# Kernel optimization log

Measured on AMD Instinct MI355X. Metric: run time of the kernel, lower is better.

The kernel has to match this reference:

```python
import jax, jax.numpy as jnp
import numpy as np

N_NODES = 50000
N_EDGES = 800000
EDGE_DIM = 64
HID = 64


def setup_inputs() -> dict:
    key = jax.random.key(0)
    ks = jax.random.split(key, 8)
    hidden_atom_emb = jax.random.normal(ks[0], (N_NODES, HID), dtype=jnp.float32)
    edge_emb = jax.random.normal(ks[1], (N_EDGES, EDGE_DIM), dtype=jnp.float32)
    edge_list = jax.random.randint(ks[2], (N_EDGES, 2), 0, N_NODES, dtype=jnp.int64)
    # filter MLP params (xavier-uniform-like scaling)
    lim1 = float(np.sqrt(6.0 / (EDGE_DIM + HID)))
    W1 = jax.random.uniform(ks[3], (EDGE_DIM, HID), minval=-lim1, maxval=lim1, dtype=jnp.float32)
    b1 = jnp.zeros((HID,), dtype=jnp.float32)
    lim2 = float(np.sqrt(6.0 / (HID + HID)))
    W2 = jax.random.uniform(ks[4], (HID, HID), minval=-lim2, maxval=lim2, dtype=jnp.float32)
    b2 = jnp.zeros((HID,), dtype=jnp.float32)
    lim3 = 1.414 * float(np.sqrt(6.0 / (HID + 1)))
    linear_coef = jax.random.uniform(ks[5], (HID, 1), minval=-lim3, maxval=lim3, dtype=jnp.float32)
    return {
        'hidden_atom_emb': hidden_atom_emb,
        'edge_emb': edge_emb,
        'W1': W1, 'b1': b1, 'W2': W2, 'b2': b2,
        'linear_coef': linear_coef,
        'edge_list': edge_list,
    }


def reference(hidden_atom_emb, edge_emb, W1, b1, W2, b2, linear_coef, edge_list):
    # filter-generating MLP: Linear + tanh, Linear
    hidden_edge_emb = jnp.tanh(edge_emb @ W1 + b1) @ W2 + b2            # [E, H]
    # gather neighbor (source) embeddings and apply continuous filter
    msg = hidden_atom_emb[edge_list[:, 1]] * hidden_edge_emb           # [E, H]
    # unnormalized edge attention (scalar per edge)
    attn = jnp.exp(msg @ linear_coef)                                   # [E, 1]
    dest = edge_list[:, 0]
    n = hidden_atom_emb.shape[0]
    # scatter-sum over neighbors (dim=1 of the sparse [N,N,H] tensors)
    num = jax.ops.segment_sum(msg * attn, dest, num_segments=n)         # [N, H]
    den = jax.ops.segment_sum(jnp.broadcast_to(attn, msg.shape), dest, num_segments=n)  # [N, H]
    return jnp.where(den > 0, num / den, num)
```

## Files before the change

### kernel.cpp

```cpp
#include <hip/hip_runtime.h>
#include <math.h>


#define TE 64
#define HID 64
#define NBLK_MLP 768

typedef __attribute__((ext_vector_type(8))) short short8;
typedef __attribute__((ext_vector_type(4))) float float4v;

__device__ __forceinline__ float fast_tanh(float x) {
    float t = __expf(2.0f * x);
    return 1.0f - 2.0f * __builtin_amdgcn_rcpf(t + 1.0f);
}

__device__ __forceinline__ void split_bf16(float x, unsigned short& hi,
                                           unsigned short& lo) {
    unsigned b = __float_as_uint(x);
    hi = (unsigned short)(b >> 16);
    float hf = __uint_as_float(b & 0xffff0000u);
    lo = (unsigned short)(__float_as_uint(x - hf) >> 16);
}

__device__ __forceinline__ void split8(const float4 u0, const float4 u1,
                                       short8& h, short8& l) {
    float xv[8] = {u0.x, u0.y, u0.z, u0.w, u1.x, u1.y, u1.z, u1.w};
    #pragma unroll
    for (int j = 0; j < 8; ++j) {
        unsigned short hi, lo;
        split_bf16(xv[j], hi, lo);
        h[j] = (short)hi; l[j] = (short)lo;
    }
}

__global__ __launch_bounds__(256) void pack_w(
    const float* __restrict__ W1, const float* __restrict__ W2,
    unsigned short* __restrict__ wpack)
{
    int t = threadIdx.x;
    for (int i = 0; i < 16; ++i) {
        int idx = t * 16 + i;
        int k = idx >> 6, f = idx & 63;
        int nt = f >> 4, n = f & 15, ks = k >> 5, q = (k >> 3) & 3, j = k & 7;
        int fi = (((nt * 2 + ks) * 4 + q) * 16 + n) * 8 + j;
        unsigned short hi, lo;
        split_bf16(W1[idx], hi, lo);
        wpack[fi] = hi; wpack[4096 + fi] = lo;
        split_bf16(W2[idx], hi, lo);
        wpack[8192 + fi] = hi; wpack[12288 + fi] = lo;
    }
}


__global__ __launch_bounds__(256) void hist_kernel(
    const int2* __restrict__ edge_list, int* __restrict__ cursor, int E)
{
    int i = blockIdx.x * blockDim.x + threadIdx.x;
    if (i < E) atomicAdd(&cursor[edge_list[i].x], 1);
}

__global__ __launch_bounds__(1024) void scanA_kernel(
    int* __restrict__ a, int* __restrict__ blocksums, int N)
{
    __shared__ int wsum[16];
    const int t = threadIdx.x;
    const int lane = t & 63, wv = t >> 6;
    int i = blockIdx.x * 1024 + t;
    int x = (i < N) ? a[i] : 0;
    int v = x;
    #pragma unroll
    for (int d = 1; d < 64; d <<= 1) {
        int y = __shfl_up(v, d);
        if (lane >= d) v += y;
    }
    if (lane == 63) wsum[wv] = v;
    __syncthreads();
    if (wv == 0 && lane < 16) {
        int s = wsum[lane];
        #pragma unroll
        for (int d = 1; d < 16; d <<= 1) {
            int y = __shfl_up(s, d);
            if (lane >= d) s += y;
        }
        wsum[lane] = s;
    }
    __syncthreads();
    int incl = v + ((wv == 0) ? 0 : wsum[wv - 1]);
    if (i < N) a[i] = incl - x;
    if (t == 1023) blocksums[blockIdx.x] = incl;
}

__global__ __launch_bounds__(64) void scanB_kernel(int* __restrict__ bs, int nb)
{
    int lane = threadIdx.x;
    int x = (lane < nb) ? bs[lane] : 0;
    int v = x;
    #pragma unroll
    for (int d = 1; d < 64; d <<= 1) {
        int y = __shfl_up(v, d);
        if (lane >= d) v += y;
    }
    if (lane < nb) bs[lane] = v - x;
}

__global__ __launch_bounds__(1024) void scanC_kernel(
    int* __restrict__ a, const int* __restrict__ blocksums, int N)
{
    int i = blockIdx.x * 1024 + threadIdx.x;
    if (i < N) a[i] += blocksums[blockIdx.x];
}

__global__ __launch_bounds__(256) void perm_kernel(
    const int2* __restrict__ edge_list, int* __restrict__ cursor,
    int* __restrict__ perm, int E)
{
    int i = blockIdx.x * blockDim.x + threadIdx.x;
    if (i < E) {
        int d = edge_list[i].x;
        int p = atomicAdd(&cursor[d], 1);
        perm[p] = i;
    }
}


__global__ __launch_bounds__(256, 3) void edge_mlp_sorted(
    const float* __restrict__ atom,
    const float* __restrict__ edge_emb,
    const unsigned short* __restrict__ wpack,
    const float* __restrict__ b1,
    const float* __restrict__ b2,
    const float* __restrict__ coef,
    const int*   __restrict__ edge_list,
    const int*   __restrict__ perm,
    float* __restrict__ num,
    float* __restrict__ den,
    int E)
{
    __shared__ __align__(16) unsigned char SH[49152];
    __shared__ float denacc[TE];
    __shared__ int   segdest[TE];

    unsigned short* B1 = (unsigned short*)SH;
    unsigned short* B2 = (unsigned short*)(SH + 16384);
    float* H1  = (float*)(SH + 32768);
    float* ACC = H1;

    const int t    = threadIdx.x;
    const int w    = t >> 6;
    const int lane = t & 63;
    const int q    = lane >> 4;
    const int n    = lane & 15;
    const int ntiles = (E + TE - 1) / TE;
    const int stride = gridDim.x;

    {
        const uint4* wp = (const uint4*)wpack;
        uint4* shw = (uint4*)SH;
        #pragma unroll
        for (int i = 0; i < 8; ++i)
            shw[t + 256 * i] = wp[t + 256 * i];
    }
    float b1v[4], b2v[4], cfv[4];
    #pragma unroll
    for (int nt = 0; nt < 4; ++nt) {
        b1v[nt] = b1[nt * 16 + n];
        b2v[nt] = b2[nt * 16 + n];
        cfv[nt] = coef[nt * 16 + n];
    }
    {
        float4 z4 = {0.f, 0.f, 0.f, 0.f};
        float4* az = (float4*)ACC;
        #pragma unroll
        for (int i = 0; i < 4; ++i) az[t + 256 * i] = z4;
        if (t < TE) denacc[t] = 0.f;
    }
    __syncthreads();

    int tt = blockIdx.x;
    int p_cur = 0, p_nxt = 0, p_nxt2 = 0;
    int2 ds_cur = make_int2(0, 0), ds_nxt = make_int2(0, 0);
    float4 rA0, rA1, rA2, rA3;
    float4 rN0 = {0,0,0,0}, rN1 = {0,0,0,0}, rN2 = {0,0,0,0}, rN3 = {0,0,0,0};
    {
        int eg = tt * TE + lane; if (eg >= E) eg = E - 1;
        p_cur = perm[eg];
        ds_cur = ((const int2*)edge_list)[p_cur];
        int pid = __shfl(p_cur, w * 16 + n);
        const float* ep = edge_emb + (size_t)pid * HID;
        rA0 = *(const float4*)(ep + q * 8);
        rA1 = *(const float4*)(ep + q * 8 + 4);
        rA2 = *(const float4*)(ep + 32 + q * 8);
        rA3 = *(const float4*)(ep + 36 + q * 8);
        int t2 = tt + stride;
        if (t2 < ntiles) {
            int eg2 = t2 * TE + lane; if (eg2 >= E) eg2 = E - 1;
            p_nxt = perm[eg2];
        }
    }

    for (; tt < ntiles; tt += stride) {
        const int eb = tt * TE;
        const bool hn = (tt + stride) < ntiles;

        int d = ds_cur.x, s = ds_cur.y;
        int dprev = __shfl_up(d, 1);
        int head = (lane == 0 || dprev != d) ? 1 : 0;
        int sv = head;
        #pragma unroll
        for (int m = 1; m < 64; m <<= 1) {
            int y = __shfl_up(sv, m);
            if (lane >= m) sv += y;
        }
        int sidx = sv - 1;
        int nseg = __shfl(sv, 63);

        int pdnd = -1;
        if (lane == 0 && eb > 0)        pdnd = edge_list[2 * perm[eb - 1]];
        if (lane == 63 && eb + TE < E)  pdnd = edge_list[2 * perm[eb + TE]];

        int seg_r[4], src_r[4];
        #pragma unroll
        for (int r = 0; r < 4; ++r) {
            int el = w * 16 + q * 4 + r;
            seg_r[r] = __shfl(sidx, el);
            src_r[r] = __shfl(s, el);
        }

        if (hn) {
            ds_nxt = ((const int2*)edge_list)[p_nxt];
            int pid2 = __shfl(p_nxt, w * 16 + n);
            const float* ep2 = edge_emb + (size_t)pid2 * HID;
            rN0 = *(const float4*)(ep2 + q * 8);
            rN1 = *(const float4*)(ep2 + q * 8 + 4);
            rN2 = *(const float4*)(ep2 + 32 + q * 8);
            rN3 = *(const float4*)(ep2 + 36 + q * 8);
            int t3 = tt + 2 * stride;
            if (t3 < ntiles) {
                int eg3 = t3 * TE + lane; if (eg3 >= E) eg3 = E - 1;
                p_nxt2 = perm[eg3];
            }
        }

        short8 a1h[2], a1l[2];
        split8(rA0, rA1, a1h[0], a1l[0]);
        split8(rA2, rA3, a1h[1], a1l[1]);
        float4v c1[4];
        #pragma unroll
        for (int i = 0; i < 4; ++i) c1[i] = (float4v){0.f, 0.f, 0.f, 0.f};
        #pragma unroll
        for (int nt = 0; nt < 4; ++nt) {
            #pragma unroll
            for (int ks = 0; ks < 2; ++ks) {
                int cb = (nt * 2 + ks) * 64 + lane;
                short8 bh = *(const short8*)&B1[cb * 8];
                short8 bl = *(const short8*)&B1[4096 + cb * 8];
                c1[nt] = __builtin_amdgcn_mfma_f32_16x16x32_bf16(a1h[ks], bh, c1[nt], 0, 0, 0);
                c1[nt] = __builtin_amdgcn_mfma_f32_16x16x32_bf16(a1h[ks], bl, c1[nt], 0, 0, 0);
                c1[nt] = __builtin_amdgcn_mfma_f32_16x16x32_bf16(a1l[ks], bh, c1[nt], 0, 0, 0);
            }
        }

        float av[4][4];
        #pragma unroll
        for (int r = 0; r < 4; ++r) {
            const float* ap = atom + (size_t)src_r[r] * HID + n;
            #pragma unroll
            for (int nt = 0; nt < 4; ++nt) av[r][nt] = ap[nt * 16];
        }

        float* h1w = H1 + w * 1024;
        #pragma unroll
        for (int nt = 0; nt < 4; ++nt) {
            int f = nt * 16 + n;
            #pragma unroll
            for (int r = 0; r < 4; ++r) {
                int m = q * 4 + r;
                h1w[m * 64 + (f ^ ((m & 7) << 3))] = fast_tanh(c1[nt][r] + b1v[nt]);
            }
        }
        asm volatile("s_waitcnt lgkmcnt(0)" ::: "memory");

        short8 a2h[2], a2l[2];
        {
            int m = n;
            #pragma unroll
            for (int ks2 = 0; ks2 < 2; ++ks2) {
                int F0 = (ks2 * 32 + q * 8) ^ ((m & 7) << 3);
                const float* sp = h1w + m * 64 + F0;
                float4 u0 = *(const float4*)&sp[0];
                float4 u1 = *(const float4*)&sp[4];
                split8(u0, u1, a2h[ks2], a2l[ks2]);
            }
        }
        {
            float4 z4 = {0.f, 0.f, 0.f, 0.f};
            float* zp = h1w + lane * 16;
            #pragma unroll
            for (int i = 0; i < 4; ++i) *(float4*)(zp + 4 * i) = z4;
        }

        float4v c2[4];
        #pragma unroll
        for (int i = 0; i < 4; ++i) c2[i] = (float4v){0.f, 0.f, 0.f, 0.f};
        #pragma unroll
        for (int nt = 0; nt < 4; ++nt) {
            #pragma unroll
            for (int ks = 0; ks < 2; ++ks) {
                int cb = (nt * 2 + ks) * 64 + lane;
                short8 bh = *(const short8*)&B2[cb * 8];
                short8 bl = *(const short8*)&B2[4096 + cb * 8];
                c2[nt] = __builtin_amdgcn_mfma_f32_16x16x32_bf16(a2h[ks], bh, c2[nt], 0, 0, 0);
                c2[nt] = __builtin_amdgcn_mfma_f32_16x16x32_bf16(a2h[ks], bl, c2[nt], 0, 0, 0);
                c2[nt] = __builtin_amdgcn_mfma_f32_16x16x32_bf16(a2l[ks], bh, c2[nt], 0, 0, 0);
            }
        }

        float msg[4][4], partial[4], at[4];
        #pragma unroll
        for (int r = 0; r < 4; ++r) {
            float p = 0.f;
            #pragma unroll
            for (int nt = 0; nt < 4; ++nt) {
                float hv = c2[nt][r] + b2v[nt];
                msg[r][nt] = av[r][nt] * hv;
                p = fmaf(msg[r][nt], cfv[nt], p);
            }
            partial[r] = p;
        }
        #pragma unroll
        for (int m = 1; m < 16; m <<= 1) {
            #pragma unroll
            for (int r = 0; r < 4; ++r)
                partial[r] += __shfl_xor(partial[r], m);
        }
        #pragma unroll
        for (int r = 0; r < 4; ++r) {
            int eg = eb + w * 16 + q * 4 + r;
            at[r] = (eg < E) ? __expf(partial[r]) : 0.f;
        }

        __syncthreads();

        if (head) segdest[sidx] = d;

        {
            int curseg = seg_r[0];
            float acc0 = msg[0][0] * at[0], acc1 = msg[0][1] * at[0];
            float acc2 = msg[0][2] * at[0], acc3 = msg[0][3] * at[0];
            float rd = at[0];
            #pragma unroll
            for (int r = 1; r < 4; ++r) {
                if (seg_r[r] == curseg) {
                    acc0 = fmaf(msg[r][0], at[r], acc0);
                    acc1 = fmaf(msg[r][1], at[r], acc1);
                    acc2 = fmaf(msg[r][2], at[r], acc2);
                    acc3 = fmaf(msg[r][3], at[r], acc3);
                    rd += at[r];
                } else {
                    float* p = &ACC[curseg * 64 + n];
                    atomicAdd(p + 0,  acc0); atomicAdd(p + 16, acc1);
                    atomicAdd(p + 32, acc2); atomicAdd(p + 48, acc3);
                    if (n == 0) atomicAdd(&denacc[curseg], rd);
                    curseg = seg_r[r];
                    acc0 = msg[r][0] * at[r]; acc1 = msg[r][1] * at[r];
                    acc2 = msg[r][2] * at[r]; acc3 = msg[r][3] * at[r];
                    rd = at[r];
                }
            }
            float* p = &ACC[curseg * 64 + n];
            atomicAdd(p + 0,  acc0); atomicAdd(p + 16, acc1);
            atomicAdd(p + 32, acc2); atomicAdd(p + 48, acc3);
            if (n == 0) atomicAdd(&denacc[curseg], rd);
        }
        __syncthreads();

        {
            int prevd = __shfl(pdnd, 0);
            int nextd = __shfl(pdnd, 63);
            int sg = t >> 2;
            int qq = t & 3;
            if (sg < nseg) {
                int d2 = segdest[sg];
                bool bnd = (sg == 0 && d2 == prevd) ||
                           (sg == nseg - 1 && d2 == nextd);
                float* np = num + (size_t)d2 * HID + qq * 16;
                const float* sp = &ACC[sg * 64 + qq * 16];
                if (bnd) {
                    #pragma unroll
                    for (int j = 0; j < 16; ++j) atomicAdd(np + j, sp[j]);
                    if (qq == 0) { atomicAdd(&den[d2], denacc[sg]); denacc[sg] = 0.f; }
                } else {
                    #pragma unroll
                    for (int j = 0; j < 4; ++j)
                        ((float4*)np)[j] = *(const float4*)(sp + 4 * j);
                    if (qq == 0) { den[d2] = denacc[sg]; denacc[sg] = 0.f; }
                }
            }
        }
        __syncthreads();

        if (hn) {
            ds_cur = ds_nxt;
            rA0 = rN0; rA1 = rN1; rA2 = rN2; rA3 = rN3;
            p_nxt = p_nxt2;
        }
    }
}

__global__ __launch_bounds__(256) void finalize_kernel(
    float* __restrict__ out, const float* __restrict__ den, int n16)
{
    int i = blockIdx.x * blockDim.x + threadIdx.x;
    if (i >= n16) return;
    float d = den[i >> 4];
    if (d > 0.f) {
        float4* p = (float4*)out + i;
        float4 v = *p;
        float r = 1.0f / d;
        v.x *= r; v.y *= r; v.z *= r; v.w *= r;
        *p = v;
    }
}

extern "C" void kernel_launch(void* const* d_in, const int* in_sizes, int n_in,
                              void* d_out, int out_size, void* d_ws, size_t ws_size,
                              hipStream_t stream) {
    const float* atom      = (const float*)d_in[0];
    const float* edge_emb  = (const float*)d_in[1];
    const float* W1        = (const float*)d_in[2];
    const float* b1        = (const float*)d_in[3];
    const float* W2        = (const float*)d_in[4];
    const float* b2        = (const float*)d_in[5];
    const float* coef      = (const float*)d_in[6];
    const int*   edge_list = (const int*)d_in[7];

    const int N = in_sizes[0] / HID;
    const int E = in_sizes[1] / HID;

    float* den       = (float*)d_ws;
    int*   cursor    = (int*)d_ws + N;
    int*   blocksums = (int*)d_ws + 2 * N;
    int*   perm      = (int*)d_ws + 2 * N + 64;
    unsigned short* wpack = (unsigned short*)((int*)d_ws + 2 * N + 64 + E);

    hipMemsetAsync(d_out, 0, (size_t)N * HID * sizeof(float), stream);
    hipMemsetAsync(d_ws, 0, (size_t)(2 * N) * sizeof(int), stream);

    pack_w<<<1, 256, 0, stream>>>(W1, W2, wpack);

    int eblk = (E + 255) / 256;
    int nb   = (N + 1023) / 1024;
    hist_kernel<<<eblk, 256, 0, stream>>>((const int2*)edge_list, cursor, E);
    scanA_kernel<<<nb, 1024, 0, stream>>>(cursor, blocksums, N);
    scanB_kernel<<<1, 64, 0, stream>>>(blocksums, nb);
    scanC_kernel<<<nb, 1024, 0, stream>>>(cursor, blocksums, N);
    perm_kernel<<<eblk, 256, 0, stream>>>((const int2*)edge_list, cursor, perm, E);

    int ntl  = (E + TE - 1) / TE;
    int nblk = ntl < NBLK_MLP ? ntl : NBLK_MLP;
    edge_mlp_sorted<<<nblk, 256, 0, stream>>>(
        atom, edge_emb, wpack, b1, b2, coef, edge_list, perm,
        (float*)d_out, den, E);

    int n16 = N * (HID / 4);
    finalize_kernel<<<(n16 + 255) / 256, 256, 0, stream>>>((float*)d_out, den, n16);
}
```

Before: 524.8 us.

## Fuse preprocessing kernels, single-block scan, and software-pipeline tile segment scan

Merges the histogram, weight packing and output zeroing into one kernel, and replaces the three-kernel block scan with a single-block looped scan. This cuts launch count and drops the separate memset of the output. In the main edge kernel, the next tile's segment scan and boundary-destination lookups are computed one iteration ahead, and atom gathers are issued earlier so their latency overlaps the MLP. Block barriers become explicit lgkmcnt waits plus s_barrier with scheduling barriers. The cost is more live registers and a serial single-block scan over all nodes.

```diff
diff --git a/kernel.cpp b/kernel.cpp
--- a/kernel.cpp
+++ b/kernel.cpp
@@ -33,13 +33,48 @@
     }
 }
 
-__global__ __launch_bounds__(256) void pack_w(
+__device__ __forceinline__ void bar_lgkm() {
+    asm volatile("s_waitcnt lgkmcnt(0)" ::: "memory");
+    __builtin_amdgcn_sched_barrier(0);
+    __builtin_amdgcn_s_barrier();
+    __builtin_amdgcn_sched_barrier(0);
+}
+
+__device__ __forceinline__ void tile_scan(int2 pr, int lane, int w, int q,
+    int& M_head, int& M_sidx, int& M_d, int& M_nseg,
+    int* M_seg, int* M_src)
+{
+    int d = pr.x, s = pr.y;
+    int dprev = __shfl_up(d, 1);
+    M_head = (lane == 0 || dprev != d) ? 1 : 0;
+    int sv = M_head;
+    #pragma unroll
+    for (int m = 1; m < 64; m <<= 1) {
+        int y = __shfl_up(sv, m);
+        if (lane >= m) sv += y;
+    }
+    M_sidx = sv - 1;
+    M_d = d;
+    M_nseg = __shfl(sv, 63);
+    #pragma unroll
+    for (int r = 0; r < 4; ++r) {
+        int el = w * 16 + q * 4 + r;
+        M_seg[r] = __shfl(M_sidx, el);
+        M_src[r] = __shfl(s, el);
+    }
+}
+
+__global__ __launch_bounds__(256) void hist_pack(
+    const int2* __restrict__ edge_list, int* __restrict__ cursor, int E,
     const float* __restrict__ W1, const float* __restrict__ W2,
-    unsigned short* __restrict__ wpack)
-{
-    int t = threadIdx.x;
-    for (int i = 0; i < 16; ++i) {
-        int idx = t * 16 + i;
+    unsigned short* __restrict__ wpack,
+    float4* __restrict__ out4, int n4)
+{
+    int i = blockIdx.x * 256 + threadIdx.x;
+    if (i < E) atomicAdd(&cursor[edge_list[i].x], 1);
+    if (i < n4) out4[i] = (float4){0.f, 0.f, 0.f, 0.f};
+    if (i < 4096) {
+        int idx = i;
         int k = idx >> 6, f = idx & 63;
         int nt = f >> 4, n = f & 15, ks = k >> 5, q = (k >> 3) & 3, j = k & 7;
         int fi = (((nt * 2 + ks) * 4 + q) * 16 + n) * 8 + j;
@@ -51,63 +86,51 @@
     }
 }
 
-
-__global__ __launch_bounds__(256) void hist_kernel(
-    const int2* __restrict__ edge_list, int* __restrict__ cursor, int E)
-{
-    int i = blockIdx.x * blockDim.x + threadIdx.x;
-    if (i < E) atomicAdd(&cursor[edge_list[i].x], 1);
-}
-
-__global__ __launch_bounds__(1024) void scanA_kernel(
-    int* __restrict__ a, int* __restrict__ blocksums, int N)
+__global__ __launch_bounds__(1024) void scan_single(int* __restrict__ a, int N)
 {
     __shared__ int wsum[16];
-    const int t = threadIdx.x;
-    const int lane = t & 63, wv = t >> 6;
-    int i = blockIdx.x * 1024 + t;
-    int x = (i < N) ? a[i] : 0;
-    int v = x;
-    #pragma unroll
-    for (int d = 1; d < 64; d <<= 1) {
-        int y = __shfl_up(v, d);
-        if (lane >= d) v += y;
-    }
-    if (lane == 63) wsum[wv] = v;
-    __syncthreads();
-    if (wv == 0 && lane < 16) {
-        int s = wsum[lane];
-        #pragma unroll
-        for (int d = 1; d < 16; d <<= 1) {
-            int y = __shfl_up(s, d);
-            if (lane >= d) s += y;
-        }
-        wsum[lane] = s;
-    }
-    __syncthreads();
-    int incl = v + ((wv == 0) ? 0 : wsum[wv - 1]);
-    if (i < N) a[i] = incl - x;
-    if (t == 1023) blocksums[blockIdx.x] = incl;
-}
-
-__global__ __launch_bounds__(64) void scanB_kernel(int* __restrict__ bs, int nb)
-{
-    int lane = threadIdx.x;
-    int x = (lane < nb) ? bs[lane] : 0;
-    int v = x;
-    #pragma unroll
-    for (int d = 1; d < 64; d <<= 1) {
-        int y = __shfl_up(v, d);
-        if (lane >= d) v += y;
-    }
-    if (lane < nb) bs[lane] = v - x;
-}
-
-__global__ __launch_bounds__(1024) void scanC_kernel(
-    int* __restrict__ a, const int* __restrict__ blocksums, int N)
-{
-    int i = blockIdx.x * 1024 + threadIdx.x;
-    if (i < N) a[i] += blocksums[blockIdx.x];
+    const int t = threadIdx.x, lane = t & 63, wv = t >> 6;
+    int running = 0;
+    const int niter = (N + 4095) / 4096;
+    for (int c = 0; c < niter; ++c) {
+        int base = (c * 1024 + t) * 4;
+        int x0 = 0, x1 = 0, x2 = 0, x3 = 0;
+        if (base + 3 < N) {
+            int4 v = *(const int4*)&a[base];
+            x0 = v.x; x1 = v.y; x2 = v.z; x3 = v.w;
+        } else {
+            if (base     < N) x0 = a[base];
+            if (base + 1 < N) x1 = a[base + 1];
+            if (base + 2 < N) x2 = a[base + 2];
+            if (base + 3 < N) x3 = a[base + 3];
+        }
+        int sum = x0 + x1 + x2 + x3;
+        int v = sum;
+        #pragma unroll
+        for (int d = 1; d < 64; d <<= 1) {
+            int y = __shfl_up(v, d);
+            if (lane >= d) v += y;
+        }
+        if (lane == 63) wsum[wv] = v;
+        __syncthreads();
+        if (wv == 0 && lane < 16) {
+            int s2 = wsum[lane];
+            #pragma unroll
+            for (int d = 1; d < 16; d <<= 1) {
+                int y = __shfl_up(s2, d);
+                if (lane >= d) s2 += y;
+            }
+            wsum[lane] = s2;
+        }
+        __syncthreads();
+        int excl = running + v - sum + (wv ? wsum[wv - 1] : 0);
+        if (base     < N) a[base]     = excl;
+        if (base + 1 < N) a[base + 1] = excl + x0;
+        if (base + 2 < N) a[base + 2] = excl + x0 + x1;
+        if (base + 3 < N) a[base + 3] = excl + x0 + x1 + x2;
+        running += wsum[15];
+        __syncthreads();
+    }
 }
 
 __global__ __launch_bounds__(256) void perm_kernel(
@@ -177,24 +200,27 @@
     __syncthreads();
 
     int tt = blockIdx.x;
-    int p_cur = 0, p_nxt = 0, p_nxt2 = 0;
-    int2 ds_cur = make_int2(0, 0), ds_nxt = make_int2(0, 0);
+    int m_head, m_sidx, m_d, m_nseg, m_seg[4], m_src[4];
+    int pdnd = -1;
+    int pA = 0;
     float4 rA0, rA1, rA2, rA3;
-    float4 rN0 = {0,0,0,0}, rN1 = {0,0,0,0}, rN2 = {0,0,0,0}, rN3 = {0,0,0,0};
     {
         int eg = tt * TE + lane; if (eg >= E) eg = E - 1;
-        p_cur = perm[eg];
-        ds_cur = ((const int2*)edge_list)[p_cur];
-        int pid = __shfl(p_cur, w * 16 + n);
+        int pc = perm[eg];
+        int2 pr = ((const int2*)edge_list)[pc];
+        int pid = __shfl(pc, w * 16 + n);
         const float* ep = edge_emb + (size_t)pid * HID;
         rA0 = *(const float4*)(ep + q * 8);
         rA1 = *(const float4*)(ep + q * 8 + 4);
         rA2 = *(const float4*)(ep + 32 + q * 8);
         rA3 = *(const float4*)(ep + 36 + q * 8);
-        int t2 = tt + stride;
-        if (t2 < ntiles) {
-            int eg2 = t2 * TE + lane; if (eg2 >= E) eg2 = E - 1;
-            p_nxt = perm[eg2];
+        int eb = tt * TE;
+        if (lane == 0 && eb > 0)       pdnd = edge_list[2 * perm[eb - 1]];
+        if (lane == 63 && eb + TE < E) pdnd = edge_list[2 * perm[eb + TE]];
+        tile_scan(pr, lane, w, q, m_head, m_sidx, m_d, m_nseg, m_seg, m_src);
+        if (tt + stride < ntiles) {
+            int eg2 = (tt + stride) * TE + lane; if (eg2 >= E) eg2 = E - 1;
+            pA = perm[eg2];
         }
     }
 
@@ -202,42 +228,31 @@
         const int eb = tt * TE;
         const bool hn = (tt + stride) < ntiles;
 
-        int d = ds_cur.x, s = ds_cur.y;
-        int dprev = __shfl_up(d, 1);
-        int head = (lane == 0 || dprev != d) ? 1 : 0;
-        int sv = head;
-        #pragma unroll
-        for (int m = 1; m < 64; m <<= 1) {
-            int y = __shfl_up(sv, m);
-            if (lane >= m) sv += y;
-        }
-        int sidx = sv - 1;
-        int nseg = __shfl(sv, 63);
-
-        int pdnd = -1;
-        if (lane == 0 && eb > 0)        pdnd = edge_list[2 * perm[eb - 1]];
-        if (lane == 63 && eb + TE < E)  pdnd = edge_list[2 * perm[eb + TE]];
-
-        int seg_r[4], src_r[4];
+        float av[4][4];
         #pragma unroll
         for (int r = 0; r < 4; ++r) {
-            int el = w * 16 + q * 4 + r;
-            seg_r[r] = __shfl(sidx, el);
-            src_r[r] = __shfl(s, el);
-        }
-
+            const float* ap = atom + (size_t)m_src[r] * HID + n;
+            #pragma unroll
+            for (int nt = 0; nt < 4; ++nt) av[r][nt] = ap[nt * 16];
+        }
+
+        int2 pr_n = make_int2(0, 0);
+        float4 rN0 = {0,0,0,0}, rN1 = {0,0,0,0}, rN2 = {0,0,0,0}, rN3 = {0,0,0,0};
+        int pB = 0, pdnd_n = -1;
         if (hn) {
-            ds_nxt = ((const int2*)edge_list)[p_nxt];
-            int pid2 = __shfl(p_nxt, w * 16 + n);
+            pr_n = ((const int2*)edge_list)[pA];
+            int pid2 = __shfl(pA, w * 16 + n);
             const float* ep2 = edge_emb + (size_t)pid2 * HID;
             rN0 = *(const float4*)(ep2 + q * 8);
             rN1 = *(const float4*)(ep2 + q * 8 + 4);
             rN2 = *(const float4*)(ep2 + 32 + q * 8);
             rN3 = *(const float4*)(ep2 + 36 + q * 8);
-            int t3 = tt + 2 * stride;
-            if (t3 < ntiles) {
-                int eg3 = t3 * TE + lane; if (eg3 >= E) eg3 = E - 1;
-                p_nxt2 = perm[eg3];
+            int ebn = (tt + stride) * TE;
+            if (lane == 0 && ebn > 0)       pdnd_n = edge_list[2 * perm[ebn - 1]];
+            if (lane == 63 && ebn + TE < E) pdnd_n = edge_list[2 * perm[ebn + TE]];
+            if (tt + 2 * stride < ntiles) {
+                int eg3 = (tt + 2 * stride) * TE + lane; if (eg3 >= E) eg3 = E - 1;
+                pB = perm[eg3];
             }
         }
 
@@ -260,13 +275,11 @@
             }
         }
 
-        float av[4][4];
-        #pragma unroll
-        for (int r = 0; r < 4; ++r) {
-            const float* ap = atom + (size_t)src_r[r] * HID + n;
-            #pragma unroll
-            for (int nt = 0; nt < 4; ++nt) av[r][nt] = ap[nt * 16];
-        }
+        int nm_head = 0, nm_sidx = 0, nm_d = 0, nm_nseg = 0;
+        int nm_seg[4] = {0,0,0,0}, nm_src[4] = {0,0,0,0};
+        if (hn)
+            tile_scan(pr_n, lane, w, q, nm_head, nm_sidx, nm_d, nm_nseg,
+                      nm_seg, nm_src);
 
         float* h1w = H1 + w * 1024;
         #pragma unroll
@@ -279,6 +292,7 @@
             }
         }
         asm volatile("s_waitcnt lgkmcnt(0)" ::: "memory");
+        __builtin_amdgcn_sched_barrier(0);
 
         short8 a2h[2], a2l[2];
         {
@@ -339,18 +353,18 @@
             at[r] = (eg < E) ? __expf(partial[r]) : 0.f;
         }
 
-        __syncthreads();
-
-        if (head) segdest[sidx] = d;
+        bar_lgkm();
+
+        if (m_head) segdest[m_sidx] = m_d;
 
         {
-            int curseg = seg_r[0];
+            int curseg = m_seg[0];
             float acc0 = msg[0][0] * at[0], acc1 = msg[0][1] * at[0];
             float acc2 = msg[0][2] * at[0], acc3 = msg[0][3] * at[0];
             float rd = at[0];
             #pragma unroll
             for (int r = 1; r < 4; ++r) {
-                if (seg_r[r] == curseg) {
+                if (m_seg[r] == curseg) {
                     acc0 = fmaf(msg[r][0], at[r], acc0);
                     acc1 = fmaf(msg[r][1], at[r], acc1);
                     acc2 = fmaf(msg[r][2], at[r], acc2);
@@ -361,7 +375,7 @@
                     atomicAdd(p + 0,  acc0); atomicAdd(p + 16, acc1);
                     atomicAdd(p + 32, acc2); atomicAdd(p + 48, acc3);
                     if (n == 0) atomicAdd(&denacc[curseg], rd);
-                    curseg = seg_r[r];
+                    curseg = m_seg[r];
                     acc0 = msg[r][0] * at[r]; acc1 = msg[r][1] * at[r];
                     acc2 = msg[r][2] * at[r]; acc3 = msg[r][3] * at[r];
                     rd = at[r];
@@ -372,17 +386,18 @@
             atomicAdd(p + 32, acc2); atomicAdd(p + 48, acc3);
             if (n == 0) atomicAdd(&denacc[curseg], rd);
         }
-        __syncthreads();
+
+        bar_lgkm();
 
         {
             int prevd = __shfl(pdnd, 0);
             int nextd = __shfl(pdnd, 63);
             int sg = t >> 2;
             int qq = t & 3;
-            if (sg < nseg) {
+            if (sg < m_nseg) {
                 int d2 = segdest[sg];
                 bool bnd = (sg == 0 && d2 == prevd) ||
-                           (sg == nseg - 1 && d2 == nextd);
+                           (sg == m_nseg - 1 && d2 == nextd);
                 float* np = num + (size_t)d2 * HID + qq * 16;
                 const float* sp = &ACC[sg * 64 + qq * 16];
                 if (bnd) {
@@ -397,12 +412,16 @@
                 }
             }
         }
-        __syncthreads();
+
+        bar_lgkm();
 
         if (hn) {
-            ds_cur = ds_nxt;
+            m_head = nm_head; m_sidx = nm_sidx; m_d = nm_d; m_nseg = nm_nseg;
+            #pragma unroll
+            for (int r = 0; r < 4; ++r) { m_seg[r] = nm_seg[r]; m_src[r] = nm_src[r]; }
+            pdnd = pdnd_n;
             rA0 = rN0; rA1 = rN1; rA2 = rN2; rA3 = rN3;
-            p_nxt = p_nxt2;
+            pA = pB;
         }
     }
 }
@@ -439,21 +458,17 @@
 
     float* den       = (float*)d_ws;
     int*   cursor    = (int*)d_ws + N;
-    int*   blocksums = (int*)d_ws + 2 * N;
     int*   perm      = (int*)d_ws + 2 * N + 64;
     unsigned short* wpack = (unsigned short*)((int*)d_ws + 2 * N + 64 + E);
 
-    hipMemsetAsync(d_out, 0, (size_t)N * HID * sizeof(float), stream);
     hipMemsetAsync(d_ws, 0, (size_t)(2 * N) * sizeof(int), stream);
 
-    pack_w<<<1, 256, 0, stream>>>(W1, W2, wpack);
-
+    int n4   = N * (HID / 4);
     int eblk = (E + 255) / 256;
-    int nb   = (N + 1023) / 1024;
-    hist_kernel<<<eblk, 256, 0, stream>>>((const int2*)edge_list, cursor, E);
-    scanA_kernel<<<nb, 1024, 0, stream>>>(cursor, blocksums, N);
-    scanB_kernel<<<1, 64, 0, stream>>>(blocksums, nb);
-    scanC_kernel<<<nb, 1024, 0, stream>>>(cursor, blocksums, N);
+    int ghp  = eblk > (n4 + 255) / 256 ? eblk : (n4 + 255) / 256;
+    hist_pack<<<ghp, 256, 0, stream>>>((const int2*)edge_list, cursor, E,
+                                       W1, W2, wpack, (float4*)d_out, n4);
+    scan_single<<<1, 1024, 0, stream>>>(cursor, N);
     perm_kernel<<<eblk, 256, 0, stream>>>((const int2*)edge_list, cursor, perm, E);
 
     int ntl  = (E + TE - 1) / TE;
@@ -462,6 +477,5 @@
         atom, edge_emb, wpack, b1, b2, coef, edge_list, perm,
         (float*)d_out, den, E);
 
-    int n16 = N * (HID / 4);
-    finalize_kernel<<<(n16 + 255) / 256, 256, 0, stream>>>((float*)d_out, den, n16);
-}
+    finalize_kernel<<<(n4 + 255) / 256, 256, 0, stream>>>((float*)d_out, den, n4);
+}
```

After: 526.1 us. Within noise of the previous version (+0.2%).
